# Kernel optimization log

Measured on AMD Instinct MI355X. Metric: run time of the kernel, lower is better.

The kernel has to match this reference:

```python
import jax, jax.numpy as jnp
import numpy as np

B, N_ELEM, N_NODES, E2 = 4096, 2048, 1024, 4096


def setup_inputs() -> dict:
    key = jax.random.key(0)
    k = jax.random.split(key, 7)
    return {
        "EA": jax.random.normal(k[0], (B, N_ELEM), dtype=jnp.float32),
        "e": jax.random.normal(k[1], (B, N_ELEM), dtype=jnp.float32),
        "q": jax.random.normal(k[2], (B, N_NODES, 2), dtype=jnp.float32),
        "r": jax.random.normal(k[3], (B, N_NODES, 2), dtype=jnp.float32),
        "vecs": jax.random.normal(k[4], (E2, 2), dtype=jnp.float32),
        "node_ids": jax.random.randint(k[5], (E2,), 0, N_NODES, dtype=jnp.int32),
        "elem_ids": jax.random.randint(k[6], (E2,), 0, N_ELEM, dtype=jnp.int32),
    }


def reference(EA, e, q, r, vecs, node_ids, elem_ids):
    # axial_forces = EA * e : [B, N_ELEM]
    axial = EA * e
    # gather per incidence entry and scale by the 2-vector: [B, E2, 2]
    contrib = axial[:, elem_ids][..., None] * vecs[None, :, :]
    n_sample, n_nodes = q.shape[0], q.shape[1]
    # scatter-add contributions into per-node residual: [B, N_NODES, 2]
    residual = jnp.zeros((n_sample, n_nodes, 2), dtype=EA.dtype)
    residual = residual.at[:, node_ids, :].add(contrib)
    residual = residual - q - r
    return jnp.mean(jnp.square(residual))
```

## Files before the change

### kernel.cpp

```cpp
#include <hip/hip_runtime.h>

#define B_SAMPLES 4096
#define N_ELEM    2048
#define N_NODES   1024
#define E2        4096
#define BLOCK     256
#define SLOTS     32
#define NODES_PER_THREAD (N_NODES / BLOCK)

#define WS_CNT_OFF   0
#define WS_ELL_OFF   4096
#define WS_PART_OFF  (4096 + SLOTS * N_NODES * 16)

__global__ __launch_bounds__(1024) void neq_setup_kernel(
    const float* __restrict__ vecs, const int* __restrict__ node_ids,
    const int* __restrict__ elem_ids, int* __restrict__ cnt,
    float4* __restrict__ ell)
{
    __shared__ int cnt_s[N_NODES];
    const int t = threadIdx.x;
    cnt_s[t] = 0;
    const int total4 = SLOTS * N_NODES;
#pragma unroll
    for (int i = 0; i < total4 / 1024; ++i)
        ell[t + i * 1024] = make_float4(0.f, 0.f, 0.f, 0.f);
    __syncthreads();

#pragma unroll
    for (int i = 0; i < E2 / 1024; ++i) {
        int j = t + i * 1024;
        int nid = node_ids[j];
        int eid = elem_ids[j];
        float2 v = ((const float2*)vecs)[j];
        int slot = atomicAdd(&cnt_s[nid], 1);
        if (slot < SLOTS) {
            float4 pk;
            pk.x = v.x;
            pk.y = v.y;
            pk.z = __int_as_float(eid);
            pk.w = 0.f;
            ell[slot * N_NODES + nid] = pk;
        }
    }
    __syncthreads();
    cnt[t] = min(cnt_s[t], SLOTS);
}

__global__ __launch_bounds__(BLOCK) void neq_main_kernel(
    const float* __restrict__ EA, const float* __restrict__ e,
    const float* __restrict__ q,  const float* __restrict__ r,
    const int* __restrict__ cnt, const float4* __restrict__ ell,
    float* __restrict__ partial)
{
    __shared__ float axial[N_ELEM];
    __shared__ float red[BLOCK / 64];

    const int b = blockIdx.x;
    const int t = threadIdx.x;

    const float4* EA4 = (const float4*)(EA + (size_t)b * N_ELEM);
    const float4* e4  = (const float4*)(e  + (size_t)b * N_ELEM);
    float4 a0 = EA4[t], a1 = EA4[t + BLOCK];
    float4 m0 = e4[t],  m1 = e4[t + BLOCK];

    int c[NODES_PER_THREAD];
    float2 qv[NODES_PER_THREAD], rv[NODES_PER_THREAD];
    const float2* q2 = (const float2*)(q + (size_t)b * N_NODES * 2);
    const float2* r2 = (const float2*)(r + (size_t)b * N_NODES * 2);
#pragma unroll
    for (int i = 0; i < NODES_PER_THREAD; ++i) {
        int n = t + i * BLOCK;
        c[i]  = cnt[n];
        qv[i] = q2[n];
        rv[i] = r2[n];
    }

    float4* ax4 = (float4*)axial;
    ax4[t]         = make_float4(a0.x * m0.x, a0.y * m0.y, a0.z * m0.z, a0.w * m0.w);
    ax4[t + BLOCK] = make_float4(a1.x * m1.x, a1.y * m1.y, a1.z * m1.z, a1.w * m1.w);
    __syncthreads();

    float accx[NODES_PER_THREAD] = {0.f, 0.f, 0.f, 0.f};
    float accy[NODES_PER_THREAD] = {0.f, 0.f, 0.f, 0.f};
    int kmax = max(max(c[0], c[1]), max(c[2], c[3]));
    for (int k = 0; k < kmax; ++k) {
        const float4* row = ell + k * N_NODES + t;
#pragma unroll
        for (int i = 0; i < NODES_PER_THREAD; ++i) {
            float4 pk = row[i * BLOCK];
            int eid  = __float_as_int(pk.z);
            float ax = axial[eid];
            accx[i] += ax * pk.x;
            accy[i] += ax * pk.y;
        }
    }

    float acc = 0.f;
#pragma unroll
    for (int i = 0; i < NODES_PER_THREAD; ++i) {
        float x = accx[i] - qv[i].x - rv[i].x;
        float y = accy[i] - qv[i].y - rv[i].y;
        acc += x * x + y * y;
    }

#pragma unroll
    for (int off = 32; off > 0; off >>= 1)
        acc += __shfl_down(acc, off, 64);
    if ((t & 63) == 0) red[t >> 6] = acc;
    __syncthreads();
    if (t == 0) partial[b] = red[0] + red[1] + red[2] + red[3];
}

__global__ __launch_bounds__(1024) void neq_reduce_kernel(
    const float* __restrict__ partial, float* __restrict__ out)
{
    __shared__ float red[1024 / 64];
    const int t = threadIdx.x;
    float acc = 0.f;
#pragma unroll
    for (int i = 0; i < B_SAMPLES / 1024; ++i) acc += partial[t + i * 1024];
#pragma unroll
    for (int off = 32; off > 0; off >>= 1)
        acc += __shfl_down(acc, off, 64);
    if ((t & 63) == 0) red[t >> 6] = acc;
    __syncthreads();
    if (t == 0) {
        float s = 0.f;
#pragma unroll
        for (int w = 0; w < 1024 / 64; ++w) s += red[w];
        const float inv_n = 1.0f / (float)((size_t)B_SAMPLES * N_NODES * 2);
        out[0] = s * inv_n;
    }
}

extern "C" void kernel_launch(void* const* d_in, const int* in_sizes, int n_in,
                              void* d_out, int out_size, void* d_ws, size_t ws_size,
                              hipStream_t stream) {
    const float* EA       = (const float*)d_in[0];
    const float* e        = (const float*)d_in[1];
    const float* q        = (const float*)d_in[2];
    const float* r        = (const float*)d_in[3];
    const float* vecs     = (const float*)d_in[4];
    const int*   node_ids = (const int*)d_in[5];
    const int*   elem_ids = (const int*)d_in[6];

    char* ws = (char*)d_ws;
    int*    cnt     = (int*)(ws + WS_CNT_OFF);
    float4* ell     = (float4*)(ws + WS_ELL_OFF);
    float*  partial = (float*)(ws + WS_PART_OFF);

    neq_setup_kernel<<<1, 1024, 0, stream>>>(vecs, node_ids, elem_ids, cnt, ell);
    neq_main_kernel<<<B_SAMPLES, BLOCK, 0, stream>>>(
        EA, e, q, r, cnt, ell, partial);
    neq_reduce_kernel<<<1, 1024, 0, stream>>>(partial, (float*)d_out);
}
```

Before: 192.7 us.

## Process four samples per block to reuse ELL loads; parallelize setup across blocks

The main kernel now handles four batch samples per block. It stores interleaved float4 axial values in shared memory so each ELL entry load and gather serves four samples. The single-block setup kernel is split into a multi-block zero kernel and a multi-block build kernel that uses global atomics, which adds a kernel launch. The cost is higher register and shared-memory use (32KB LDS), fewer blocks, and strided scalar loads for EA and e.

```diff
diff --git a/kernel.cpp b/kernel.cpp
--- a/kernel.cpp
+++ b/kernel.cpp
@@ -6,101 +6,98 @@
 #define E2        4096
 #define BLOCK     256
 #define SLOTS     32
-#define NODES_PER_THREAD (N_NODES / BLOCK)
+#define S         4
+#define MAIN_BLOCKS (B_SAMPLES / S)
 
 #define WS_CNT_OFF   0
 #define WS_ELL_OFF   4096
 #define WS_PART_OFF  (4096 + SLOTS * N_NODES * 16)
 
-__global__ __launch_bounds__(1024) void neq_setup_kernel(
+__global__ __launch_bounds__(BLOCK) void neq_zero_kernel(
+    float4* __restrict__ ell, int* __restrict__ cnt)
+{
+    const int i = blockIdx.x * BLOCK + threadIdx.x;
+    ell[i] = make_float4(0.f, 0.f, 0.f, 0.f);
+    if (i < N_NODES) cnt[i] = 0;
+}
+
+__global__ __launch_bounds__(BLOCK) void neq_build_kernel(
     const float* __restrict__ vecs, const int* __restrict__ node_ids,
     const int* __restrict__ elem_ids, int* __restrict__ cnt,
     float4* __restrict__ ell)
 {
-    __shared__ int cnt_s[N_NODES];
-    const int t = threadIdx.x;
-    cnt_s[t] = 0;
-    const int total4 = SLOTS * N_NODES;
-#pragma unroll
-    for (int i = 0; i < total4 / 1024; ++i)
-        ell[t + i * 1024] = make_float4(0.f, 0.f, 0.f, 0.f);
-    __syncthreads();
-
-#pragma unroll
-    for (int i = 0; i < E2 / 1024; ++i) {
-        int j = t + i * 1024;
-        int nid = node_ids[j];
-        int eid = elem_ids[j];
-        float2 v = ((const float2*)vecs)[j];
-        int slot = atomicAdd(&cnt_s[nid], 1);
-        if (slot < SLOTS) {
-            float4 pk;
-            pk.x = v.x;
-            pk.y = v.y;
-            pk.z = __int_as_float(eid);
-            pk.w = 0.f;
-            ell[slot * N_NODES + nid] = pk;
-        }
+    const int j = blockIdx.x * BLOCK + threadIdx.x;
+    int nid = node_ids[j];
+    int eid = elem_ids[j];
+    float2 v = ((const float2*)vecs)[j];
+    int slot = atomicAdd(&cnt[nid], 1);
+    if (slot < SLOTS) {
+        ell[slot * N_NODES + nid] = make_float4(v.x, v.y, __int_as_float(eid), 0.f);
     }
-    __syncthreads();
-    cnt[t] = min(cnt_s[t], SLOTS);
 }
 
-__global__ __launch_bounds__(BLOCK) void neq_main_kernel(
+__global__ __launch_bounds__(BLOCK, 4) void neq_main_kernel(
     const float* __restrict__ EA, const float* __restrict__ e,
     const float* __restrict__ q,  const float* __restrict__ r,
     const int* __restrict__ cnt, const float4* __restrict__ ell,
     float* __restrict__ partial)
 {
-    __shared__ float axial[N_ELEM];
+    __shared__ float4 axial4[N_ELEM];
     __shared__ float red[BLOCK / 64];
 
-    const int b = blockIdx.x;
+    const int b0 = blockIdx.x * S;
     const int t = threadIdx.x;
 
-    const float4* EA4 = (const float4*)(EA + (size_t)b * N_ELEM);
-    const float4* e4  = (const float4*)(e  + (size_t)b * N_ELEM);
-    float4 a0 = EA4[t], a1 = EA4[t + BLOCK];
-    float4 m0 = e4[t],  m1 = e4[t + BLOCK];
-
-    int c[NODES_PER_THREAD];
-    float2 qv[NODES_PER_THREAD], rv[NODES_PER_THREAD];
-    const float2* q2 = (const float2*)(q + (size_t)b * N_NODES * 2);
-    const float2* r2 = (const float2*)(r + (size_t)b * N_NODES * 2);
 #pragma unroll
-    for (int i = 0; i < NODES_PER_THREAD; ++i) {
-        int n = t + i * BLOCK;
-        c[i]  = cnt[n];
-        qv[i] = q2[n];
-        rv[i] = r2[n];
+    for (int i = 0; i < N_ELEM / BLOCK; ++i) {
+        int eid = t + i * BLOCK;
+        float4 p;
+        const float* EAp = EA + (size_t)b0 * N_ELEM + eid;
+        const float* ep  = e  + (size_t)b0 * N_ELEM + eid;
+        p.x = EAp[0 * N_ELEM] * ep[0 * N_ELEM];
+        p.y = EAp[1 * N_ELEM] * ep[1 * N_ELEM];
+        p.z = EAp[2 * N_ELEM] * ep[2 * N_ELEM];
+        p.w = EAp[3 * N_ELEM] * ep[3 * N_ELEM];
+        axial4[eid] = p;
     }
 
-    float4* ax4 = (float4*)axial;
-    ax4[t]         = make_float4(a0.x * m0.x, a0.y * m0.y, a0.z * m0.z, a0.w * m0.w);
-    ax4[t + BLOCK] = make_float4(a1.x * m1.x, a1.y * m1.y, a1.z * m1.z, a1.w * m1.w);
+    int c0 = min(cnt[t], SLOTS);
+    int c1 = min(cnt[t + 256], SLOTS);
+    int c2 = min(cnt[t + 512], SLOTS);
+    int c3 = min(cnt[t + 768], SLOTS);
+    int kmax = max(max(c0, c1), max(c2, c3));
     __syncthreads();
 
-    float accx[NODES_PER_THREAD] = {0.f, 0.f, 0.f, 0.f};
-    float accy[NODES_PER_THREAD] = {0.f, 0.f, 0.f, 0.f};
-    int kmax = max(max(c[0], c[1]), max(c[2], c[3]));
+    float accx[4][S] = {};
+    float accy[4][S] = {};
     for (int k = 0; k < kmax; ++k) {
         const float4* row = ell + k * N_NODES + t;
 #pragma unroll
-        for (int i = 0; i < NODES_PER_THREAD; ++i) {
+        for (int i = 0; i < 4; ++i) {
             float4 pk = row[i * BLOCK];
-            int eid  = __float_as_int(pk.z);
-            float ax = axial[eid];
-            accx[i] += ax * pk.x;
-            accy[i] += ax * pk.y;
+            int eid = __float_as_int(pk.z);
+            float4 ax = axial4[eid];
+            accx[i][0] += ax.x * pk.x;  accy[i][0] += ax.x * pk.y;
+            accx[i][1] += ax.y * pk.x;  accy[i][1] += ax.y * pk.y;
+            accx[i][2] += ax.z * pk.x;  accy[i][2] += ax.z * pk.y;
+            accx[i][3] += ax.w * pk.x;  accy[i][3] += ax.w * pk.y;
         }
     }
 
     float acc = 0.f;
 #pragma unroll
-    for (int i = 0; i < NODES_PER_THREAD; ++i) {
-        float x = accx[i] - qv[i].x - rv[i].x;
-        float y = accy[i] - qv[i].y - rv[i].y;
-        acc += x * x + y * y;
+    for (int s = 0; s < S; ++s) {
+        const float2* q2 = (const float2*)(q + (size_t)(b0 + s) * N_NODES * 2);
+        const float2* r2 = (const float2*)(r + (size_t)(b0 + s) * N_NODES * 2);
+#pragma unroll
+        for (int i = 0; i < 4; ++i) {
+            int n = t + i * BLOCK;
+            float2 qv = q2[n];
+            float2 rv = r2[n];
+            float x = accx[i][s] - qv.x - rv.x;
+            float y = accy[i][s] - qv.y - rv.y;
+            acc += x * x + y * y;
+        }
     }
 
 #pragma unroll
@@ -108,7 +105,7 @@
         acc += __shfl_down(acc, off, 64);
     if ((t & 63) == 0) red[t >> 6] = acc;
     __syncthreads();
-    if (t == 0) partial[b] = red[0] + red[1] + red[2] + red[3];
+    if (t == 0) partial[blockIdx.x] = red[0] + red[1] + red[2] + red[3];
 }
 
 __global__ __launch_bounds__(1024) void neq_reduce_kernel(
@@ -116,9 +113,7 @@
 {
     __shared__ float red[1024 / 64];
     const int t = threadIdx.x;
-    float acc = 0.f;
-#pragma unroll
-    for (int i = 0; i < B_SAMPLES / 1024; ++i) acc += partial[t + i * 1024];
+    float acc = partial[t];
 #pragma unroll
     for (int off = 32; off > 0; off >>= 1)
         acc += __shfl_down(acc, off, 64);
@@ -149,8 +144,10 @@
     float4* ell     = (float4*)(ws + WS_ELL_OFF);
     float*  partial = (float*)(ws + WS_PART_OFF);
 
-    neq_setup_kernel<<<1, 1024, 0, stream>>>(vecs, node_ids, elem_ids, cnt, ell);
-    neq_main_kernel<<<B_SAMPLES, BLOCK, 0, stream>>>(
+    neq_zero_kernel<<<(SLOTS * N_NODES) / BLOCK, BLOCK, 0, stream>>>(ell, cnt);
+    neq_build_kernel<<<E2 / BLOCK, BLOCK, 0, stream>>>(
+        vecs, node_ids, elem_ids, cnt, ell);
+    neq_main_kernel<<<MAIN_BLOCKS, BLOCK, 0, stream>>>(
         EA, e, q, r, cnt, ell, partial);
     neq_reduce_kernel<<<1, 1024, 0, stream>>>(partial, (float*)d_out);
 }
```

Measured after the change: 162.4 us. -15.7%, faster.
